# Performance work log

Measured on AMD Instinct MI355X. Metric: run time of the kernel, lower is better.

## Reference

```python
import jax, jax.numpy as jnp
import numpy as np

K = 8192  # num_embeddings
D = 512   # embedding_dim
BETA = 0.25


def setup_inputs() -> dict:
    key = jax.random.key(0)
    k1, k2, k3 = jax.random.split(key, 3)
    B, T = 64, 512
    latents = jax.random.normal(k1, (B, T, D), dtype=jnp.float32)
    # nn.Embedding weight initialized uniform(-1/K, 1/K)
    emb = jax.random.uniform(k2, (K, D), dtype=jnp.float32, minval=-1.0 / K, maxval=1.0 / K)
    gold_encoding_inds = jax.random.randint(k3, (B * T, 1), 0, K, dtype=jnp.int64 if jax.config.jax_enable_x64 else jnp.int32)
    return {"gold_encoding_inds": gold_encoding_inds, "latents": latents, "epc": 1, "emb": emb}


def reference(gold_encoding_inds, latents, epc, emb):
    B, T, _ = latents.shape
    flat = latents.reshape(B * T, D)  # [N, D]
    # squared euclidean distance to every codebook entry: [N, K]
    dist = (jnp.sum(flat * flat, axis=1, keepdims=True)
            + jnp.sum(emb * emb, axis=1)
            - 2.0 * jnp.matmul(flat, emb.T))
    encoding_inds = jnp.argmin(dist, axis=1)[:, None]  # [N, 1]
    # one-hot @ emb  ==  gather rows of emb
    quantized = emb[encoding_inds[:, 0]].reshape(B, T, D)
    # per-position MSE over the feature dim
    commitment_loss = jnp.mean((jax.lax.stop_gradient(quantized) - latents) ** 2, axis=-1)
    embedding_loss = jnp.mean((quantized - jax.lax.stop_gradient(latents)) ** 2, axis=-1)
    vq_loss = embedding_loss + BETA * commitment_loss  # [B, T]
    # straight-through estimator
    quantized = latents + jax.lax.stop_gradient(quantized - latents)
    correct = jnp.sum(gold_encoding_inds == encoding_inds)
    total = jnp.asarray(gold_encoding_inds.shape[0], dtype=jnp.int32)
    return quantized, vq_loss, encoding_inds.T, (correct, total)
```

## Files before the change

### kernel.cpp

```cpp
#include <hip/hip_runtime.h>
#include <math.h>

#define N_ROWS 32768
#define KCB    8192
#define DIM    512
#define BETA   0.25f
#define MARGIN 2e-3f
#define FLAG_SLACK 1e-4f
#define CAND_CAP 256

typedef __attribute__((ext_vector_type(4))) float  f32x4;
typedef __attribute__((ext_vector_type(4))) int    i32x4;
typedef __attribute__((ext_vector_type(8))) int    i32x8;

__device__ __forceinline__ unsigned short f2h(float x) {
    _Float16 h = (_Float16)x;
    return *(unsigned short*)&h;
}
__device__ __forceinline__ float h2f(unsigned short u) {
    _Float16 h = *(_Float16*)&u;
    return (float)h;
}

#define SQ_BLOCKS ((N_ROWS + KCB) / 8)
__global__ __launch_bounds__(256) void pre_kernel(
        const float* __restrict__ lat, const float* __restrict__ emb,
        float* __restrict__ row_sq, float* __restrict__ emb_sq,
        unsigned char* __restrict__ latq, unsigned char* __restrict__ embq,
        int* __restrict__ counter) {
    if (blockIdx.x < SQ_BLOCKS) {
#pragma clang fp contract(off)
        if (blockIdx.x == 0 && threadIdx.x == 0) *counter = 0;
        const int w    = threadIdx.x >> 6;
        const int lane = threadIdx.x & 63;
        const int half = lane >> 5;
        const int L    = lane & 31;
        const int b    = L >> 3, j = L & 7;
        const int row  = blockIdx.x * 8 + w * 2 + half;
        const float* p = (row < N_ROWS) ? (lat + (size_t)row * DIM)
                                        : (emb + (size_t)(row - N_ROWS) * DIM);
        const float* q = p + 128 * b + j;
        float a0 = q[0];
        float r  = a0 * a0;
        for (int i = 1; i < 16; ++i) {
            float a = q[8 * i];
            float s = a * a;
            r = r + s;
        }
        r = r + __shfl_xor(r, 1);
        r = r + __shfl_xor(r, 2);
        r = r + __shfl_xor(r, 4);
        r = r + __shfl_xor(r, 8);
        r = r + __shfl_xor(r, 16);
        if (L == 0) {
            if (row < N_ROWS) row_sq[row] = r;
            else              emb_sq[row - N_ROWS] = r;
        }
    } else {
        const size_t NL8 = (size_t)N_ROWS * DIM / 8;
        const size_t NE8 = (size_t)KCB * DIM / 8;
        size_t g = (size_t)(blockIdx.x - SQ_BLOCKS) * 256 + threadIdx.x;
        const float* src; unsigned char* dst; size_t i; float sc;
        if (g < NL8)            { src = lat; dst = latq; i = g;       sc = 1.0f; }
        else if (g < NL8 + NE8) { src = emb; dst = embq; i = g - NL8; sc = 8192.0f; }
        else return;
        float4 v0 = ((const float4*)src)[2 * i];
        float4 v1 = ((const float4*)src)[2 * i + 1];
        int lo = __builtin_amdgcn_cvt_pk_fp8_f32(v0.x * sc, v0.y * sc, 0,  false);
        lo     = __builtin_amdgcn_cvt_pk_fp8_f32(v0.z * sc, v0.w * sc, lo, true);
        int hi = __builtin_amdgcn_cvt_pk_fp8_f32(v1.x * sc, v1.y * sc, 0,  false);
        hi     = __builtin_amdgcn_cvt_pk_fp8_f32(v1.z * sc, v1.w * sc, hi, true);
        ((int2*)dst)[i] = make_int2(lo, hi);
    }
}

__device__ __forceinline__ void load16_to_lds(const void* g, void* l) {
    __builtin_amdgcn_global_load_lds(
        (const __attribute__((address_space(1))) unsigned int*)g,
        (__attribute__((address_space(3))) unsigned int*)l, 16, 0, 0);
}

__global__ __launch_bounds__(256, 3) void gemm_kernel(
        const unsigned char* __restrict__ latq,
        const unsigned char* __restrict__ embq,
        const float* __restrict__ emb_sq,
        unsigned int* __restrict__ packed) {
    __shared__ unsigned char Ac[128 * 128];
    __shared__ unsigned char Br[128 * 128];

    const int tid   = threadIdx.x;
    const int w     = tid >> 6;
    const int lane  = tid & 63;
    const int q     = lane >> 4;
    const int m16   = lane & 15;
    const int row0  = blockIdx.x * 128;
    const int code0 = blockIdx.y * 128;
    const int wc    = 64 * (w >> 1);
    const int rbase = 64 * (w & 1);

    int soff[8];
#pragma unroll
    for (int i = 0; i < 8; ++i) {
        int cid   = w * 8 + i;
        int h     = cid & 15;
        int base0 = (cid < 16) ? code0 : row0;
        soff[i] = (base0 + h * 8 + (lane >> 3)) * DIM
                + (((lane & 7) ^ (lane >> 3)) << 4);
    }

    f32x4 acc[4][4];
#pragma unroll
    for (int r = 0; r < 4; ++r)
#pragma unroll
        for (int c = 0; c < 4; ++c) acc[r][c] = (f32x4){0.f, 0.f, 0.f, 0.f};

    const int sw = (m16 & 7) << 4;

    for (int k0 = 0; k0 < DIM; k0 += 128) {
#pragma unroll
        for (int i = 0; i < 8; ++i) {
            int cid = w * 8 + i;
            const unsigned char* g = ((cid < 16) ? embq : latq) + soff[i] + k0;
            unsigned char* l = ((cid < 16) ? Ac : Br) + (cid & 15) * 1024;
            load16_to_lds(g, l);
        }
        __syncthreads();

        i32x8 af[4];
#pragma unroll
        for (int r = 0; r < 4; ++r) {
            int roff = (wc + 16 * r + m16) * 128;
            i32x4 lo = *(const i32x4*)&Ac[roff + ((q * 32) ^ sw)];
            i32x4 hi = *(const i32x4*)&Ac[roff + ((q * 32 + 16) ^ sw)];
            af[r] = (i32x8){lo[0], lo[1], lo[2], lo[3],
                            hi[0], hi[1], hi[2], hi[3]};
        }
#pragma unroll
        for (int c = 0; c < 4; ++c) {
            int roff = (rbase + 16 * c + m16) * 128;
            i32x4 lo = *(const i32x4*)&Br[roff + ((q * 32) ^ sw)];
            i32x4 hi = *(const i32x4*)&Br[roff + ((q * 32 + 16) ^ sw)];
            i32x8 bv = (i32x8){lo[0], lo[1], lo[2], lo[3],
                               hi[0], hi[1], hi[2], hi[3]};
#pragma unroll
            for (int r = 0; r < 4; ++r)
                acc[r][c] = __builtin_amdgcn_mfma_scale_f32_16x16x128_f8f6f4(
                    af[r], bv, acc[r][c],
                    0, 0,
                    0, 0x7F7F7F7F,
                    0, 0x7F7F7F7F);
        }
        __syncthreads();
    }

    float sev[4][4];
#pragma unroll
    for (int r = 0; r < 4; ++r)
#pragma unroll
        for (int reg = 0; reg < 4; ++reg)
            sev[r][reg] = emb_sq[code0 + wc + 16 * r + 4 * q + reg];

    const float inv = 1.0f / 4096.0f;
#pragma unroll
    for (int c = 0; c < 4; ++c) {
        unsigned pk[4];
#pragma unroll
        for (int r = 0; r < 4; ++r) {
            float s0 = sev[r][0] - acc[r][c][0] * inv;
            float s1 = sev[r][1] - acc[r][c][1] * inv;
            float s2 = sev[r][2] - acc[r][c][2] * inv;
            float s3 = sev[r][3] - acc[r][c][3] * inv;
            float mn = fminf(fminf(s0, s1), fminf(s2, s3));
            mn = fminf(mn, __shfl_xor(mn, 16));
            mn = fminf(mn, __shfl_xor(mn, 32));
            float t = mn + MARGIN;
            unsigned nib = (s0 <= t ? 1u : 0u) | (s1 <= t ? 2u : 0u)
                         | (s2 <= t ? 4u : 0u) | (s3 <= t ? 8u : 0u);
            nib <<= (4 * q);
            nib |= (unsigned)__shfl_xor((int)nib, 16);
            nib |= (unsigned)__shfl_xor((int)nib, 32);
            pk[r] = ((unsigned)f2h(mn)) | (nib << 16);
        }
        if (lane < 16) {
            int grow = row0 + rbase + 16 * c + m16;
            int base = (code0 + wc) >> 4;
            *(uint4*)&packed[(size_t)grow * 512 + base] =
                make_uint4(pk[0], pk[1], pk[2], pk[3]);
        }
    }
}

__global__ __launch_bounds__(256) void argmin_out_kernel(
        const float* __restrict__ lat, const float* __restrict__ emb,
        const float* __restrict__ row_sq, const float* __restrict__ emb_sq,
        const unsigned int* __restrict__ packed,
        const int* __restrict__ gold,
        float* __restrict__ out, int* __restrict__ counter) {
    __shared__ float xs[4][DIM];
    __shared__ int   s_cnt[4];
    __shared__ int   s_list[4][CAND_CAP];
    const int w    = threadIdx.x >> 6;
    const int lane = threadIdx.x & 63;
    const int row  = blockIdx.x * 4 + w;

    {
        const float4* xp = (const float4*)(lat + (size_t)row * DIM);
        ((float4*)xs[w])[lane]      = xp[lane];
        ((float4*)xs[w])[lane + 64] = xp[lane + 64];
    }
    const float sx = row_sq[row];
    const float* xw = xs[w];

    unsigned u[8];
    {
        const uint4* tb = (const uint4*)(packed + (size_t)row * 512 + lane * 8);
        uint4 v0 = tb[0], v1 = tb[1];
        u[0] = v0.x; u[1] = v0.y; u[2] = v0.z; u[3] = v0.w;
        u[4] = v1.x; u[5] = v1.y; u[6] = v1.z; u[7] = v1.w;
    }
    float tm[8];
#pragma unroll
    for (int j = 0; j < 8; ++j) tm[j] = h2f((unsigned short)(u[j] & 0xFFFFu));
    float m = tm[0];
#pragma unroll
    for (int j = 1; j < 8; ++j) m = fminf(m, tm[j]);
#pragma unroll
    for (int off = 1; off < 64; off <<= 1)
        m = fminf(m, __shfl_xor(m, off));
    const float thresh = m + (MARGIN + FLAG_SLACK);

    if (lane == 0) s_cnt[w] = 0;
    __syncthreads();
#pragma unroll
    for (int j = 0; j < 8; ++j) {
        if (tm[j] <= thresh) {
            int g = lane * 8 + j;
            unsigned bm = u[j] >> 16;
            while (bm) {
                int b = __ffs(bm) - 1;
                bm &= bm - 1;
                int pos = atomicAdd(&s_cnt[w], 1);
                if (pos < CAND_CAP) s_list[w][pos] = g * 16 + b;
            }
        }
    }
    __syncthreads();
    const int cnt = min(s_cnt[w], CAND_CAP);

    float bd = INFINITY;
    int   bi = 0x7fffffff;
    for (int base = 0; base < cnt; base += 64) {
        int ci = base + lane;
        float dvl = INFINITY;
        int   cl  = 0x7fffffff;
        if (ci < cnt) {
            int code = s_list[w][ci];
            const float* ep = emb + (size_t)code * DIM;
            float acc = 0.0f;
            for (int d = 0; d < DIM; d += 8) {
                float ev[8], xv[8];
#pragma unroll
                for (int t = 0; t < 8; ++t) { ev[t] = ep[d + t]; xv[t] = xw[d + t]; }
#pragma unroll
                for (int t = 0; t < 8; ++t) acc = fmaf(xv[t], ev[t], acc);
            }
            float a = sx + emb_sq[code];
            dvl = a - 2.0f * acc;
            cl  = code;
        }
        if (dvl < bd || (dvl == bd && cl < bi)) { bd = dvl; bi = cl; }
    }
#pragma unroll
    for (int off = 1; off < 64; off <<= 1) {
        float od = __shfl_xor(bd, off);
        int   oi = __shfl_xor(bi, off);
        if (od < bd || (od == bd && oi < bi)) { bd = od; bi = oi; }
    }
    const int idx = bi;

    const float4* e4 = (const float4*)(emb + (size_t)idx * DIM);
    float4*       q4 = (float4*)(out + (size_t)row * DIM);
    q4[lane]      = e4[lane];
    q4[lane + 64] = e4[lane + 64];

    float r = 0.0f;
    if (lane < 32) {
        const int b = lane >> 3, j = lane & 7;
        const float* ep = emb + (size_t)idx * DIM + b * 128 + j;
        const float* xp = xw + b * 128 + j;
        for (int i = 0; i < 16; ++i) {
            float dq = ep[8 * i] - xp[8 * i];
            float s  = dq * dq;
            r = (i == 0) ? s : (r + s);
        }
    }
    for (int mm = 1; mm <= 16; mm <<= 1) {
        float o = __shfl_xor(r, mm);
        r = r + o;
    }
    if (lane == 0) {
        float mean = r * (1.0f / 512.0f);
        float v    = mean + 0.25f * mean;
        out[(size_t)N_ROWS * DIM + row]          = v;
        out[(size_t)N_ROWS * DIM + N_ROWS + row] = (float)idx;
        if (gold[row] == idx) atomicAdd(counter, 1);
    }
}

__global__ void tail_kernel(const int* __restrict__ counter,
                            float* __restrict__ out) {
    if (threadIdx.x == 0 && blockIdx.x == 0) {
        const size_t off = (size_t)N_ROWS * DIM + 2 * (size_t)N_ROWS;
        out[off]     = (float)(*counter);
        out[off + 1] = (float)N_ROWS;
    }
}

__global__ __launch_bounds__(256) void sq_kernel(
        const float* __restrict__ lat, const float* __restrict__ emb,
        float* __restrict__ row_sq, float* __restrict__ emb_sq) {
#pragma clang fp contract(off)
    const int w    = threadIdx.x >> 6;
    const int lane = threadIdx.x & 63;
    const int half = lane >> 5;
    const int L    = lane & 31;
    const int b    = L >> 3, j = L & 7;
    const int row  = blockIdx.x * 8 + w * 2 + half;
    if (row >= N_ROWS + KCB) return;
    const float* p = (row < N_ROWS) ? (lat + (size_t)row * DIM)
                                    : (emb + (size_t)(row - N_ROWS) * DIM);
    const float* q = p + 128 * b + j;
    float a0 = q[0];
    float r  = a0 * a0;
    for (int i = 1; i < 16; ++i) {
        float a = q[8 * i];
        float s = a * a;
        r = r + s;
    }
    r = r + __shfl_xor(r, 1);
    r = r + __shfl_xor(r, 2);
    r = r + __shfl_xor(r, 4);
    r = r + __shfl_xor(r, 8);
    r = r + __shfl_xor(r, 16);
    if (L == 0) {
        if (row < N_ROWS) row_sq[row] = r;
        else              emb_sq[row - N_ROWS] = r;
    }
}

#define BM 64
#define BK 128
#define BD 32
__global__ __launch_bounds__(256) void dist_kernel(
        const float* __restrict__ lat, const float* __restrict__ emb,
        const float* __restrict__ row_sq, const float* __restrict__ emb_sq,
        int* __restrict__ enc) {
    __shared__ float xsh[BD][BM];
    __shared__ float esh[BD][BK];
    const int tid  = threadIdx.x;
    const int trow = tid >> 4;
    const int tcol = tid & 15;
    const int row0 = blockIdx.x * BM;
    float bd[4]; int bi[4];
    for (int i = 0; i < 4; ++i) { bd[i] = INFINITY; bi[i] = 0; }
    float sx[4];
    for (int i = 0; i < 4; ++i) sx[i] = row_sq[row0 + 4 * trow + i];
    for (int kt = 0; kt < KCB; kt += BK) {
        float acc[4][8] = {};
        for (int d0 = 0; d0 < DIM; d0 += BD) {
            for (int f = tid; f < BM * BD / 4; f += 256) {
                int r = f >> 3, c4 = f & 7;
                float4 v = *(const float4*)(lat + (size_t)(row0 + r) * DIM + d0 + 4 * c4);
                xsh[4 * c4 + 0][r] = v.x; xsh[4 * c4 + 1][r] = v.y;
                xsh[4 * c4 + 2][r] = v.z; xsh[4 * c4 + 3][r] = v.w;
            }
            for (int f = tid; f < BK * BD / 4; f += 256) {
                int r = f >> 3, c4 = f & 7;
                float4 v = *(const float4*)(emb + (size_t)(kt + r) * DIM + d0 + 4 * c4);
                esh[4 * c4 + 0][r] = v.x; esh[4 * c4 + 1][r] = v.y;
                esh[4 * c4 + 2][r] = v.z; esh[4 * c4 + 3][r] = v.w;
            }
            __syncthreads();
            for (int dd = 0; dd < BD; ++dd) {
                float4 xv  = *(const float4*)&xsh[dd][4 * trow];
                float4 ev0 = *(const float4*)&esh[dd][8 * tcol];
                float4 ev1 = *(const float4*)&esh[dd][8 * tcol + 4];
                float xr[4] = { xv.x, xv.y, xv.z, xv.w };
                float ec[8] = { ev0.x, ev0.y, ev0.z, ev0.w, ev1.x, ev1.y, ev1.z, ev1.w };
                for (int r = 0; r < 4; ++r)
                    for (int c = 0; c < 8; ++c)
                        acc[r][c] = fmaf(xr[r], ec[c], acc[r][c]);
            }
            __syncthreads();
        }
        for (int c = 0; c < 8; ++c) {
            int   code = kt + 8 * tcol + c;
            float se   = emb_sq[code];
            for (int r = 0; r < 4; ++r) {
                float a  = sx[r] + se;
                float dv = a - 2.0f * acc[r][c];
                if (dv < bd[r]) { bd[r] = dv; bi[r] = code; }
            }
        }
    }
    for (int off = 1; off < 16; off <<= 1) {
        for (int r = 0; r < 4; ++r) {
            float od = __shfl_xor(bd[r], off);
            int   oi = __shfl_xor(bi[r], off);
            if (od < bd[r] || (od == bd[r] && oi < bi[r])) { bd[r] = od; bi[r] = oi; }
        }
    }
    if (tcol == 0)
        for (int r = 0; r < 4; ++r)
            enc[row0 + 4 * trow + r] = bi[r];
}

__global__ void out_kernel(const float* __restrict__ lat,
                           const float* __restrict__ emb,
                           const int* __restrict__ gold,
                           const int* __restrict__ enc,
                           float* __restrict__ out,
                           int* __restrict__ counter) {
#pragma clang fp contract(off)
    const int gid  = blockIdx.x * blockDim.x + threadIdx.x;
    const int row  = gid >> 6;
    const int lane = threadIdx.x & 63;
    if (row >= N_ROWS) return;
    const int idx = enc[row];
    const float4* e4 = (const float4*)(emb + (size_t)idx * DIM);
    float4*       q4 = (float4*)(out + (size_t)row * DIM);
    q4[lane]      = e4[lane];
    q4[lane + 64] = e4[lane + 64];
    float r = 0.0f;
    if (lane < 32) {
        const int b = lane >> 3, j = lane & 7;
        const float* ep = emb + (size_t)idx * DIM + b * 128 + j;
        const float* xp = lat + (size_t)row * DIM + b * 128 + j;
        for (int i = 0; i < 16; ++i) {
            float dq = ep[8 * i] - xp[8 * i];
            float s  = dq * dq;
            r = (i == 0) ? s : (r + s);
        }
    }
    for (int m = 1; m <= 16; m <<= 1) {
        float o = __shfl_xor(r, m);
        r = r + o;
    }
    if (lane == 0) {
        float mean = r * (1.0f / 512.0f);
        float v    = mean + 0.25f * mean;
        out[(size_t)N_ROWS * DIM + row]          = v;
        out[(size_t)N_ROWS * DIM + N_ROWS + row] = (float)idx;
        if (gold[row] == idx) atomicAdd(counter, 1);
    }
}

extern "C" void kernel_launch(void* const* d_in, const int* in_sizes, int n_in,
                              void* d_out, int out_size, void* d_ws, size_t ws_size,
                              hipStream_t stream) {
    (void)in_sizes; (void)n_in; (void)out_size;
    const int*   gold = (const int*)d_in[0];
    const float* lat  = (const float*)d_in[1];
    const float* emb  = (const float*)d_in[3];
    float* out = (float*)d_out;

    const size_t SZ_LATQ = (size_t)N_ROWS * DIM;
    const size_t SZ_EMBQ = (size_t)KCB * DIM;
    const size_t SZ_PK   = (size_t)N_ROWS * 512 * 4;
    const size_t SZ_SMALL = (size_t)N_ROWS * 4 + (size_t)KCB * 4 + 256;
    const size_t NEEDED = SZ_LATQ + SZ_EMBQ + SZ_PK + SZ_SMALL;

    if (ws_size >= NEEDED) {
        unsigned char* w8 = (unsigned char*)d_ws;
        unsigned char* latq    = w8;
        unsigned char* embq    = w8 + SZ_LATQ;
        unsigned int*  packed  = (unsigned int*)(w8 + SZ_LATQ + SZ_EMBQ);
        float*         row_sq  = (float*)(w8 + SZ_LATQ + SZ_EMBQ + SZ_PK);
        float*         emb_sq  = row_sq + N_ROWS;
        int*           counter = (int*)(emb_sq + KCB);

        const int pre_blocks = SQ_BLOCKS + (N_ROWS + KCB) * (DIM / 8) / 256;
        pre_kernel<<<pre_blocks, 256, 0, stream>>>(
            lat, emb, row_sq, emb_sq, latq, embq, counter);
        dim3 ggrid(N_ROWS / 128, KCB / 128);
        gemm_kernel<<<ggrid, 256, 0, stream>>>(latq, embq, emb_sq, packed);
        argmin_out_kernel<<<N_ROWS / 4, 256, 0, stream>>>(
            lat, emb, row_sq, emb_sq, packed, gold, out, counter);
        tail_kernel<<<1, 64, 0, stream>>>(counter, out);
    } else {
        float* row_sq  = (float*)d_ws;
        float* emb_sq  = row_sq + N_ROWS;
        int*   enc     = (int*)(emb_sq + KCB);
        int*   counter = enc + N_ROWS;
        hipMemsetAsync(counter, 0, sizeof(int), stream);
        sq_kernel<<<(N_ROWS + KCB) / 8, 256, 0, stream>>>(lat, emb, row_sq, emb_sq);
        dist_kernel<<<N_ROWS / BM, 256, 0, stream>>>(lat, emb, row_sq, emb_sq, enc);
        out_kernel<<<N_ROWS / 4, 256, 0, stream>>>(lat, emb, gold, enc, out, counter);
        tail_kernel<<<1, 64, 0, stream>>>(counter, out);
    }
}
```

Before: 580.9 us.

## Double-buffer GEMM LDS tiles and remap blocks for XCD/L2 locality

Turns the FP8 GEMM K-loop into a two-stage pipeline: the LDS tiles are double-buffered, so the next 128-wide K slice is prefetched with global_load_lds while MFMAs run on the current one, synchronised by explicit vmcnt waits and s_barrier. The 2D grid also becomes a 1D grid with a swizzled block-to-tile mapping that groups row and code tiles per XCD and supertile, aiming for better L2 reuse of the latent and codebook slices. LDS use doubles to 64 KB per block, and launch bounds drop occupancy from 3 to 2 blocks per CU, which costs latency hiding in exchange.

```diff
diff --git a/kernel.cpp b/kernel.cpp
--- a/kernel.cpp
+++ b/kernel.cpp
@@ -80,21 +80,29 @@
         (__attribute__((address_space(3))) unsigned int*)l, 16, 0, 0);
 }
 
-__global__ __launch_bounds__(256, 3) void gemm_kernel(
+__global__ __launch_bounds__(256, 2) void gemm_kernel(
         const unsigned char* __restrict__ latq,
         const unsigned char* __restrict__ embq,
         const float* __restrict__ emb_sq,
         unsigned int* __restrict__ packed) {
-    __shared__ unsigned char Ac[128 * 128];
-    __shared__ unsigned char Br[128 * 128];
+    __shared__ unsigned char Ac[2][128 * 128];
+    __shared__ unsigned char Br[2][128 * 128];
 
     const int tid   = threadIdx.x;
     const int w     = tid >> 6;
     const int lane  = tid & 63;
     const int q     = lane >> 4;
     const int m16   = lane & 15;
-    const int row0  = blockIdx.x * 128;
-    const int code0 = blockIdx.y * 128;
+
+    const int b   = blockIdx.x;
+    const int l   = (b & 7) * 2048 + (b >> 3);
+    const int st  = l >> 9;
+    const int r2  = l & 511;
+    const int rg  = st & 7;
+    const int cg  = st >> 3;
+    const int row0  = (rg * 32 + (r2 & 31)) * 128;
+    const int code0 = (cg * 16 + (r2 >> 5)) * 128;
+
     const int wc    = 64 * (w >> 1);
     const int rbase = 64 * (w & 1);
 
@@ -108,6 +116,19 @@
                 + (((lane & 7) ^ (lane >> 3)) << 4);
     }
 
+#define STAGE(bsel, k0)                                                     \
+    do {                                                                    \
+        _Pragma("unroll")                                                   \
+        for (int i = 0; i < 8; ++i) {                                       \
+            int cid = w * 8 + i;                                            \
+            const unsigned char* g =                                        \
+                ((cid < 16) ? embq : latq) + soff[i] + (k0);                \
+            unsigned char* dst = ((cid < 16) ? &Ac[bsel][0] : &Br[bsel][0]) \
+                               + (cid & 15) * 1024;                         \
+            load16_to_lds(g, dst);                                          \
+        }                                                                   \
+    } while (0)
+
     f32x4 acc[4][4];
 #pragma unroll
     for (int r = 0; r < 4; ++r)
@@ -116,30 +137,32 @@
 
     const int sw = (m16 & 7) << 4;
 
-    for (int k0 = 0; k0 < DIM; k0 += 128) {
-#pragma unroll
-        for (int i = 0; i < 8; ++i) {
-            int cid = w * 8 + i;
-            const unsigned char* g = ((cid < 16) ? embq : latq) + soff[i] + k0;
-            unsigned char* l = ((cid < 16) ? Ac : Br) + (cid & 15) * 1024;
-            load16_to_lds(g, l);
-        }
-        __syncthreads();
+    STAGE(0, 0);
+
+#pragma unroll
+    for (int t = 0; t < 4; ++t) {
+        const int bsel = t & 1;
+        if (t < 3) STAGE((t + 1) & 1, (t + 1) * 128);
+        __builtin_amdgcn_sched_barrier(0);
+        if (t < 3) { asm volatile("s_waitcnt vmcnt(8)" ::: "memory"); }
+        else       { asm volatile("s_waitcnt vmcnt(0)" ::: "memory"); }
+        __builtin_amdgcn_s_barrier();
+        __builtin_amdgcn_sched_barrier(0);
 
         i32x8 af[4];
 #pragma unroll
         for (int r = 0; r < 4; ++r) {
             int roff = (wc + 16 * r + m16) * 128;
-            i32x4 lo = *(const i32x4*)&Ac[roff + ((q * 32) ^ sw)];
-            i32x4 hi = *(const i32x4*)&Ac[roff + ((q * 32 + 16) ^ sw)];
+            i32x4 lo = *(const i32x4*)&Ac[bsel][roff + ((q * 32) ^ sw)];
+            i32x4 hi = *(const i32x4*)&Ac[bsel][roff + ((q * 32 + 16) ^ sw)];
             af[r] = (i32x8){lo[0], lo[1], lo[2], lo[3],
                             hi[0], hi[1], hi[2], hi[3]};
         }
 #pragma unroll
         for (int c = 0; c < 4; ++c) {
             int roff = (rbase + 16 * c + m16) * 128;
-            i32x4 lo = *(const i32x4*)&Br[roff + ((q * 32) ^ sw)];
-            i32x4 hi = *(const i32x4*)&Br[roff + ((q * 32 + 16) ^ sw)];
+            i32x4 lo = *(const i32x4*)&Br[bsel][roff + ((q * 32) ^ sw)];
+            i32x4 hi = *(const i32x4*)&Br[bsel][roff + ((q * 32 + 16) ^ sw)];
             i32x8 bv = (i32x8){lo[0], lo[1], lo[2], lo[3],
                                hi[0], hi[1], hi[2], hi[3]};
 #pragma unroll
@@ -150,8 +173,11 @@
                     0, 0x7F7F7F7F,
                     0, 0x7F7F7F7F);
         }
-        __syncthreads();
-    }
+        __builtin_amdgcn_sched_barrier(0);
+        __builtin_amdgcn_s_barrier();
+        __builtin_amdgcn_sched_barrier(0);
+    }
+#undef STAGE
 
     float sev[4][4];
 #pragma unroll
@@ -482,8 +508,8 @@
         const int pre_blocks = SQ_BLOCKS + (N_ROWS + KCB) * (DIM / 8) / 256;
         pre_kernel<<<pre_blocks, 256, 0, stream>>>(
             lat, emb, row_sq, emb_sq, latq, embq, counter);
-        dim3 ggrid(N_ROWS / 128, KCB / 128);
-        gemm_kernel<<<ggrid, 256, 0, stream>>>(latq, embq, emb_sq, packed);
+        gemm_kernel<<<(N_ROWS / 128) * (KCB / 128), 256, 0, stream>>>(
+            latq, embq, emb_sq, packed);
         argmin_out_kernel<<<N_ROWS / 4, 256, 0, stream>>>(
             lat, emb, row_sq, emb_sq, packed, gold, out, counter);
         tail_kernel<<<1, 64, 0, stream>>>(counter, out);
```

After: 538.8 us. 1.08x faster.
